# Kernel optimization log

Measured on AMD Instinct MI355X. Metric: run time of the kernel, lower is better.

The kernel has to match this reference:

```python
import jax, jax.numpy as jnp
import numpy as np

DIM = 2048
N_HEADS = 16
HEAD_DIM = DIM // N_HEADS
WINDOW = 256
B, S = 2, 2048


def setup_inputs() -> dict:
    key = jax.random.key(0)
    kx, kq, kk, kv, ko = jax.random.split(key, 5)
    bound = 1.0 / np.sqrt(DIM)  # nn.Linear default init range
    x = jax.random.normal(kx, (B, S, DIM), dtype=jnp.float32)
    wq = jax.random.uniform(kq, (DIM, DIM), jnp.float32, -bound, bound)
    wk = jax.random.uniform(kk, (DIM, DIM), jnp.float32, -bound, bound)
    wv = jax.random.uniform(kv, (DIM, DIM), jnp.float32, -bound, bound)
    wo = jax.random.uniform(ko, (DIM, DIM), jnp.float32, -bound, bound)
    return {"x": x, "wq": wq, "wk": wk, "wv": wv, "wo": wo}


def reference(x, wq, wk, wv, wo):
    b, s, d = x.shape
    scale = HEAD_DIM ** -0.5
    # projections (torch Linear: y = x @ W.T)
    q = (x @ wq.T).reshape(b, s, N_HEADS, HEAD_DIM)
    k = (x @ wk.T).reshape(b, s, N_HEADS, HEAD_DIM)
    v = (x @ wv.T).reshape(b, s, N_HEADS, HEAD_DIM)
    # scores: [b, h, i, j]
    scores = jnp.einsum("bihd,bjhd->bhij", q, k) * scale
    # faithful mask: (all-ones, window cleared, then triu(1)) == mask iff j - i > window//2
    idx = jnp.arange(s)
    mask = (idx[None, :] - idx[:, None]) > (WINDOW // 2)  # [s, s] bool, True = masked
    scores = jnp.where(mask[None, None, :, :], -jnp.inf, scores)
    attn = jax.nn.softmax(scores, axis=-1)
    out = jnp.einsum("bhij,bjhd->bihd", attn, v).reshape(b, s, d)
    return out @ wo.T
```

## Files before the change

### kernel.cpp

```cpp
#include <hip/hip_runtime.h>
#include <stdint.h>
#include <stddef.h>

#define DIMN 2048
#define NH 16
#define HD 128
#define SEQ 2048
#define WIN 128

typedef __attribute__((ext_vector_type(4))) float f32x4;
typedef __attribute__((ext_vector_type(8))) short bf16x8;
typedef __attribute__((ext_vector_type(4))) int i32x4;

#define AS1 __attribute__((address_space(1)))
#define AS3 __attribute__((address_space(3)))

__device__ __forceinline__ unsigned short f2bf(float f) {
  union { float f; unsigned u; } v; v.f = f;
  unsigned r = v.u + 0x7FFFu + ((v.u >> 16) & 1u);
  return (unsigned short)(r >> 16);
}

__global__ void cast_bf16_kernel(const float* __restrict__ src,
                                 unsigned short* __restrict__ dst, int n4) {
  int i = blockIdx.x * blockDim.x + threadIdx.x;
  const int stride = gridDim.x * blockDim.x;
  for (; i < n4; i += stride) {
    float4 v = ((const float4*)src)[i];
    ushort4 o;
    o.x = f2bf(v.x); o.y = f2bf(v.y); o.z = f2bf(v.z); o.w = f2bf(v.w);
    ((ushort4*)dst)[i] = o;
  }
}

__global__ void cast4_bf16_kernel(const float* __restrict__ s0, const float* __restrict__ s1,
                                  const float* __restrict__ s2, const float* __restrict__ s3,
                                  unsigned short* __restrict__ dst, int n4) {
  const float* s = (blockIdx.y == 0) ? s0 : (blockIdx.y == 1) ? s1 : (blockIdx.y == 2) ? s2 : s3;
  unsigned short* d = dst + (size_t)blockIdx.y * 4194304;
  int i = blockIdx.x * blockDim.x + threadIdx.x;
  const int stride = gridDim.x * blockDim.x;
  for (; i < n4; i += stride) {
    float4 v = ((const float4*)s)[i];
    ushort4 o;
    o.x = f2bf(v.x); o.y = f2bf(v.y); o.z = f2bf(v.z); o.w = f2bf(v.w);
    ((ushort4*)d)[i] = o;
  }
}

__device__ __forceinline__ void gemm_mainloop_g128(
    const unsigned short* __restrict__ A, const unsigned short* __restrict__ B,
    int m0, int n0, unsigned short* As, unsigned short* Bs, f32x4 acc[4][4]) {
  const int t = threadIdx.x, lane = t & 63, wid = t >> 6;
  const int c = lane & 15, g = lane >> 4;
  const int wr = wid >> 1, wc = wid & 1;

  const int srow = wid * 32 + (lane >> 3);
  const int gslot = (lane & 7) ^ (lane >> 3);
  const unsigned short* ga = A + (size_t)(m0 + srow) * DIMN + gslot * 8;
  const unsigned short* gb = B + (size_t)(n0 + srow) * DIMN + gslot * 8;
  unsigned short* la = As + (size_t)(wid * 32) * 64;
  unsigned short* lb = Bs + (size_t)(wid * 32) * 64;

  const int swc = c & 7;

  for (int k0 = 0; k0 < DIMN; k0 += 64) {
    __syncthreads();
#pragma unroll
    for (int i = 0; i < 4; ++i) {
      __builtin_amdgcn_global_load_lds(
          (const AS1 unsigned*)(ga + (size_t)i * 8 * DIMN + k0),
          (AS3 unsigned*)(la + i * 8 * 64), 16, 0, 0);
      __builtin_amdgcn_global_load_lds(
          (const AS1 unsigned*)(gb + (size_t)i * 8 * DIMN + k0),
          (AS3 unsigned*)(lb + i * 8 * 64), 16, 0, 0);
    }
    __syncthreads();
#pragma unroll
    for (int kk = 0; kk < 2; ++kk) {
      bf16x8 af[4], bfv[4];
#pragma unroll
      for (int mi = 0; mi < 4; ++mi)
        af[mi] = *(const bf16x8*)&As[(wr * 64 + mi * 16 + c) * 64 +
                                     (((kk * 4 + g) ^ swc) * 8)];
#pragma unroll
      for (int ni = 0; ni < 4; ++ni)
        bfv[ni] = *(const bf16x8*)&Bs[(wc * 64 + ni * 16 + c) * 64 +
                                      (((kk * 4 + g) ^ swc) * 8)];
#pragma unroll
      for (int mi = 0; mi < 4; ++mi)
#pragma unroll
        for (int ni = 0; ni < 4; ++ni)
          acc[mi][ni] = __builtin_amdgcn_mfma_f32_16x16x32_bf16(
              af[mi], bfv[ni], acc[mi][ni], 0, 0, 0);
    }
  }
}

__global__ __launch_bounds__(256, 3) void gemm_qkv_kernel(
    const unsigned short* __restrict__ Xb,
    const unsigned short* __restrict__ Wq,
    const unsigned short* __restrict__ Wk,
    const unsigned short* __restrict__ Wv,
    unsigned short* __restrict__ Qb,
    unsigned short* __restrict__ Kb,
    unsigned short* __restrict__ Vt) {
  __shared__ __attribute__((aligned(16))) unsigned short As[128 * 64];
  __shared__ __attribute__((aligned(16))) unsigned short Bs[128 * 64];
  const int z = blockIdx.z;
  const unsigned short* W = (z == 0) ? Wq : (z == 1) ? Wk : Wv;
  const int m0 = blockIdx.y * 128, n0 = blockIdx.x * 128;

  f32x4 acc[4][4];
  const f32x4 zv = {0.f, 0.f, 0.f, 0.f};
#pragma unroll
  for (int i = 0; i < 4; ++i)
#pragma unroll
    for (int j = 0; j < 4; ++j) acc[i][j] = zv;

  gemm_mainloop_g128(Xb, W, m0, n0, As, Bs, acc);

  const int lane = threadIdx.x & 63, wid = threadIdx.x >> 6;
  const int c = lane & 15, g = lane >> 4;
  const int wr = wid >> 1, wc = wid & 1;
  unsigned short* Out01 = (z == 0) ? Qb : Kb;
#pragma unroll
  for (int mi = 0; mi < 4; ++mi) {
#pragma unroll
    for (int ni = 0; ni < 4; ++ni) {
      const int mrow = m0 + wr * 64 + mi * 16 + g * 4;
      const int ncol = n0 + wc * 64 + ni * 16 + c;
      const int h = ncol >> 7, d = ncol & 127;
      const int b = mrow >> 11, s = mrow & 2047;
      if (z < 2) {
#pragma unroll
        for (int j = 0; j < 4; ++j)
          Out01[((size_t)(b * NH + h) * SEQ + s + j) * HD + d] =
              f2bf(acc[mi][ni][j]);
      } else {
        ushort4 pk;
        pk.x = f2bf(acc[mi][ni][0]); pk.y = f2bf(acc[mi][ni][1]);
        pk.z = f2bf(acc[mi][ni][2]); pk.w = f2bf(acc[mi][ni][3]);
        *(ushort4*)&Vt[((size_t)(b * NH + h) * HD + d) * SEQ + s] = pk;
      }
    }
  }
}

__global__ __launch_bounds__(256, 3) void gemm_out_kernel(
    const unsigned short* __restrict__ Ab,
    const unsigned short* __restrict__ Wo,
    float* __restrict__ Cf) {
  __shared__ __attribute__((aligned(16))) unsigned short As[128 * 64];
  __shared__ __attribute__((aligned(16))) unsigned short Bs[128 * 64];
  const int m0 = blockIdx.y * 128, n0 = blockIdx.x * 128;

  f32x4 acc[4][4];
  const f32x4 zv = {0.f, 0.f, 0.f, 0.f};
#pragma unroll
  for (int i = 0; i < 4; ++i)
#pragma unroll
    for (int j = 0; j < 4; ++j) acc[i][j] = zv;

  gemm_mainloop_g128(Ab, Wo, m0, n0, As, Bs, acc);

  const int lane = threadIdx.x & 63, wid = threadIdx.x >> 6;
  const int c = lane & 15, g = lane >> 4;
  const int wr = wid >> 1, wc = wid & 1;
#pragma unroll
  for (int mi = 0; mi < 4; ++mi) {
#pragma unroll
    for (int ni = 0; ni < 4; ++ni) {
      const int mrow = m0 + wr * 64 + mi * 16 + g * 4;
      const int ncol = n0 + wc * 64 + ni * 16 + c;
#pragma unroll
      for (int j = 0; j < 4; ++j)
        Cf[(size_t)(mrow + j) * DIMN + ncol] = acc[mi][ni][j];
    }
  }
}

__global__ __launch_bounds__(256, 2) void attn_kernel(
    const unsigned short* __restrict__ Qg,
    const unsigned short* __restrict__ Kg,
    const unsigned short* __restrict__ Vtg,
    unsigned short* __restrict__ Og) {
  __shared__ __attribute__((aligned(16))) unsigned short Ks[2][64 * 128];
  __shared__ __attribute__((aligned(16))) unsigned short Vs[2][128 * 64];
  __shared__ __attribute__((aligned(16))) unsigned short Ps[4 * 32 * 64];

  const int bh = blockIdx.x;
  const int yy = blockIdx.y;
  const int qt = (yy < 8) ? yy : 23 - yy;
  const int q0 = qt * 128;
  const int t = threadIdx.x, wid = t >> 6, lane = t & 63;
  const int c = lane & 15, g = lane >> 4;
  const int swc = c & 7;

  const unsigned short* Kbh = Kg + (size_t)bh * SEQ * HD;
  const unsigned short* Vbh = Vtg + (size_t)bh * HD * SEQ;

  bf16x8 qf[2][4];
#pragma unroll
  for (int mi = 0; mi < 2; ++mi) {
    const unsigned short* qb =
        Qg + ((size_t)bh * SEQ + q0 + wid * 32 + mi * 16 + c) * HD + g * 8;
#pragma unroll
    for (int kk = 0; kk < 4; ++kk) qf[mi][kk] = *(const bf16x8*)(qb + kk * 32);
  }

  f32x4 o[2][8];
  const f32x4 zv = {0.f, 0.f, 0.f, 0.f};
#pragma unroll
  for (int mi = 0; mi < 2; ++mi)
#pragma unroll
    for (int ni = 0; ni < 8; ++ni) o[mi][ni] = zv;
  float M[2][4], L[2][4];
#pragma unroll
  for (int mi = 0; mi < 2; ++mi)
#pragma unroll
    for (int j = 0; j < 4; ++j) { M[mi][j] = -1e30f; L[mi][j] = 0.f; }

  const int ntA = (q0 + 256) >> 6;
  const int nt = (ntA < (SEQ >> 6)) ? ntA : (SEQ >> 6);
  const float kl2e = 0.08838834764831845f * 1.4426950408889634f;

  const int kswz = (t & 15) ^ ((t >> 4) & 7);
  const int vswz = (t & 7) ^ ((t >> 3) & 7);
  const int kgo = (t >> 4) * HD + (t & 15) * 8;
  const int klo = (t >> 4) * 128 + kswz * 8;
  const int vlo = (t >> 3) * 64 + vswz * 8;
  const size_t vgo = (size_t)(t >> 3) * SEQ + (t & 7) * 8;

  i32x4 kc[4], vc[4];
#pragma unroll
  for (int r = 0; r < 4; ++r) {
    kc[r] = *(const i32x4*)(Kbh + (size_t)r * 16 * HD + kgo);
    vc[r] = *(const i32x4*)(Vbh + (size_t)r * 32 * SEQ + vgo);
  }
#pragma unroll
  for (int r = 0; r < 4; ++r) {
    *(i32x4*)&Ks[0][r * 2048 + klo] = kc[r];
    *(i32x4*)&Vs[0][r * 2048 + vlo] = vc[r];
  }
  if (nt > 1) {
#pragma unroll
    for (int r = 0; r < 4; ++r) {
      kc[r] = *(const i32x4*)(Kbh + (size_t)(64 + r * 16) * HD + kgo);
      vc[r] = *(const i32x4*)(Vbh + (size_t)r * 32 * SEQ + 64 + vgo);
    }
  }
  __syncthreads();

  int cur = 0;
  for (int tt = 0; tt < nt; ++tt) {
    const int j0 = tt * 64;
    if (tt + 1 < nt) {
#pragma unroll
      for (int r = 0; r < 4; ++r) {
        *(i32x4*)&Ks[cur ^ 1][r * 2048 + klo] = kc[r];
        *(i32x4*)&Vs[cur ^ 1][r * 2048 + vlo] = vc[r];
      }
      if (tt + 2 < nt) {
        const int j2 = j0 + 128;
#pragma unroll
        for (int r = 0; r < 4; ++r) {
          kc[r] = *(const i32x4*)(Kbh + (size_t)(j2 + r * 16) * HD + kgo);
          vc[r] = *(const i32x4*)(Vbh + (size_t)r * 32 * SEQ + j2 + vgo);
        }
      }
    }
    const unsigned short* Kc = Ks[cur];
    const unsigned short* Vc = Vs[cur];

    f32x4 sc[2][4];
#pragma unroll
    for (int mi = 0; mi < 2; ++mi)
#pragma unroll
      for (int ni = 0; ni < 4; ++ni) sc[mi][ni] = zv;
    __builtin_amdgcn_s_setprio(1);
#pragma unroll
    for (int kk = 0; kk < 4; ++kk) {
#pragma unroll
      for (int ni = 0; ni < 4; ++ni) {
        const bf16x8 kf =
            *(const bf16x8*)&Kc[(ni * 16 + c) * 128 + ((kk * 4 + g) ^ swc) * 8];
        sc[0][ni] = __builtin_amdgcn_mfma_f32_16x16x32_bf16(qf[0][kk], kf, sc[0][ni], 0, 0, 0);
        sc[1][ni] = __builtin_amdgcn_mfma_f32_16x16x32_bf16(qf[1][kk], kf, sc[1][ni], 0, 0, 0);
      }
    }
    __builtin_amdgcn_s_setprio(0);

    if (j0 - q0 >= 128) {
#pragma unroll
      for (int mi = 0; mi < 2; ++mi)
#pragma unroll
        for (int ni = 0; ni < 4; ++ni) {
          const int jg = j0 + ni * 16 + c;
#pragma unroll
          for (int j = 0; j < 4; ++j) {
            const int ig = q0 + wid * 32 + mi * 16 + g * 4 + j;
            if (jg > ig + WIN) sc[mi][ni][j] = -3.0e38f;
          }
        }
    }

    float tmax[2][4], dmax = -3.0e38f;
#pragma unroll
    for (int mi = 0; mi < 2; ++mi)
#pragma unroll
      for (int j = 0; j < 4; ++j) {
        float mx = fmaxf(fmaxf(sc[mi][0][j], sc[mi][1][j]),
                         fmaxf(sc[mi][2][j], sc[mi][3][j]));
        mx = fmaxf(mx, __shfl_xor(mx, 1));
        mx = fmaxf(mx, __shfl_xor(mx, 2));
        mx = fmaxf(mx, __shfl_xor(mx, 4));
        mx = fmaxf(mx, __shfl_xor(mx, 8));
        tmax[mi][j] = mx;
        dmax = fmaxf(dmax, mx - M[mi][j]);
      }
    if (__any(dmax > 64.f)) {
#pragma unroll
      for (int mi = 0; mi < 2; ++mi)
#pragma unroll
        for (int j = 0; j < 4; ++j) {
          const float nm = fmaxf(M[mi][j], tmax[mi][j]);
          const float al = __builtin_amdgcn_exp2f((M[mi][j] - nm) * kl2e);
          M[mi][j] = nm;
          L[mi][j] *= al;
#pragma unroll
          for (int ni = 0; ni < 8; ++ni) o[mi][ni][j] *= al;
        }
    }

#pragma unroll
    for (int mi = 0; mi < 2; ++mi) {
      float rs0 = 0.f, rs1 = 0.f, rs2 = 0.f, rs3 = 0.f;
#pragma unroll
      for (int ni = 0; ni < 4; ++ni)
#pragma unroll
        for (int j = 0; j < 4; ++j) {
          const float p = __builtin_amdgcn_exp2f((sc[mi][ni][j] - M[mi][j]) * kl2e);
          if (j == 0) rs0 += p; else if (j == 1) rs1 += p;
          else if (j == 2) rs2 += p; else rs3 += p;
          const int prow = mi * 16 + g * 4 + j;
          Ps[wid * 2048 + prow * 64 + ((2 * ni + (c >> 3)) ^ (prow & 7)) * 8 + (c & 7)] =
              f2bf(p);
        }
      L[mi][0] += rs0; L[mi][1] += rs1; L[mi][2] += rs2; L[mi][3] += rs3;
    }

    __builtin_amdgcn_s_setprio(1);
#pragma unroll
    for (int kk2 = 0; kk2 < 2; ++kk2) {
      bf16x8 pf[2];
#pragma unroll
      for (int mi = 0; mi < 2; ++mi)
        pf[mi] = *(const bf16x8*)&Ps[wid * 2048 + (mi * 16 + c) * 64 +
                                     ((kk2 * 4 + g) ^ swc) * 8];
#pragma unroll
      for (int ni = 0; ni < 8; ++ni) {
        const bf16x8 vf =
            *(const bf16x8*)&Vc[(ni * 16 + c) * 64 + ((kk2 * 4 + g) ^ swc) * 8];
        o[0][ni] = __builtin_amdgcn_mfma_f32_16x16x32_bf16(pf[0], vf, o[0][ni], 0, 0, 0);
        o[1][ni] = __builtin_amdgcn_mfma_f32_16x16x32_bf16(pf[1], vf, o[1][ni], 0, 0, 0);
      }
    }
    __builtin_amdgcn_s_setprio(0);

    __syncthreads();
    cur ^= 1;
  }

  const int b = bh >> 4, h = bh & 15;
#pragma unroll
  for (int mi = 0; mi < 2; ++mi)
#pragma unroll
    for (int j = 0; j < 4; ++j) {
      float s = L[mi][j];
      s += __shfl_xor(s, 1);
      s += __shfl_xor(s, 2);
      s += __shfl_xor(s, 4);
      s += __shfl_xor(s, 8);
      const float inv = 1.0f / s;
      const int srow = q0 + wid * 32 + mi * 16 + g * 4 + j;
      unsigned short* orow = Og + (size_t)(b * SEQ + srow) * DIMN + h * HD;
#pragma unroll
      for (int ni = 0; ni < 8; ++ni) orow[ni * 16 + c] = f2bf(o[mi][ni][j] * inv);
    }
}

extern "C" void kernel_launch(void* const* d_in, const int* in_sizes, int n_in,
                              void* d_out, int out_size, void* d_ws, size_t ws_size,
                              hipStream_t stream) {
  (void)in_sizes; (void)n_in; (void)out_size; (void)ws_size;
  const float* x  = (const float*)d_in[0];
  const float* wq = (const float*)d_in[1];
  const float* wk = (const float*)d_in[2];
  const float* wv = (const float*)d_in[3];
  const float* wo = (const float*)d_in[4];
  float* out = (float*)d_out;

  unsigned short* xb  = (unsigned short*)d_ws;
  unsigned short* wqb = xb  + (size_t)8388608;
  unsigned short* wkb = wqb + (size_t)4194304;
  unsigned short* wvb = wkb + (size_t)4194304;
  unsigned short* wob = wvb + (size_t)4194304;
  unsigned short* Qb  = wob + (size_t)4194304;
  unsigned short* Kb  = Qb  + (size_t)8388608;
  unsigned short* Vt  = Kb  + (size_t)8388608;
  unsigned short* Ab  = Vt  + (size_t)8388608;

  cast_bf16_kernel<<<dim3(1024), dim3(256), 0, stream>>>(x, xb, 2097152);
  cast4_bf16_kernel<<<dim3(512, 4), dim3(256), 0, stream>>>(wq, wk, wv, wo, wqb, 1048576);

  gemm_qkv_kernel<<<dim3(16, 32, 3), dim3(256), 0, stream>>>(xb, wqb, wkb, wvb, Qb, Kb, Vt);
  attn_kernel<<<dim3(32, 16), dim3(256), 0, stream>>>(Qb, Kb, Vt, Ab);
  gemm_out_kernel<<<dim3(16, 32), dim3(256), 0, stream>>>(Ab, wob, out);
}
```

Before: 379.3 us.

## Transpose attention MFMA operands so each lane owns a query row; merge cast kernels

Result: faster. 345.5 us (-8.9%).

```diff
diff --git a/kernel.cpp b/kernel.cpp
--- a/kernel.cpp
+++ b/kernel.cpp
@@ -21,30 +21,25 @@
   return (unsigned short)(r >> 16);
 }
 
-__global__ void cast_bf16_kernel(const float* __restrict__ src,
-                                 unsigned short* __restrict__ dst, int n4) {
+__global__ void cast_all_kernel(const float* __restrict__ x,
+                                const float* __restrict__ wq, const float* __restrict__ wk,
+                                const float* __restrict__ wv, const float* __restrict__ wo,
+                                unsigned short* __restrict__ dst) {
+  const int y = blockIdx.y;
+  const float* s;
+  if (y < 2) s = x + (size_t)y * 4194304;
+  else if (y == 2) s = wq;
+  else if (y == 3) s = wk;
+  else if (y == 4) s = wv;
+  else s = wo;
+  ushort4* d = (ushort4*)dst + (size_t)y * 1048576;
   int i = blockIdx.x * blockDim.x + threadIdx.x;
   const int stride = gridDim.x * blockDim.x;
-  for (; i < n4; i += stride) {
-    float4 v = ((const float4*)src)[i];
-    ushort4 o;
-    o.x = f2bf(v.x); o.y = f2bf(v.y); o.z = f2bf(v.z); o.w = f2bf(v.w);
-    ((ushort4*)dst)[i] = o;
-  }
-}
-
-__global__ void cast4_bf16_kernel(const float* __restrict__ s0, const float* __restrict__ s1,
-                                  const float* __restrict__ s2, const float* __restrict__ s3,
-                                  unsigned short* __restrict__ dst, int n4) {
-  const float* s = (blockIdx.y == 0) ? s0 : (blockIdx.y == 1) ? s1 : (blockIdx.y == 2) ? s2 : s3;
-  unsigned short* d = dst + (size_t)blockIdx.y * 4194304;
-  int i = blockIdx.x * blockDim.x + threadIdx.x;
-  const int stride = gridDim.x * blockDim.x;
-  for (; i < n4; i += stride) {
+  for (; i < 1048576; i += stride) {
     float4 v = ((const float4*)s)[i];
     ushort4 o;
     o.x = f2bf(v.x); o.y = f2bf(v.y); o.z = f2bf(v.z); o.w = f2bf(v.w);
-    ((ushort4*)d)[i] = o;
+    d[i] = o;
   }
 }
 
@@ -215,11 +210,8 @@
   for (int mi = 0; mi < 2; ++mi)
 #pragma unroll
     for (int ni = 0; ni < 8; ++ni) o[mi][ni] = zv;
-  float M[2][4], L[2][4];
-#pragma unroll
-  for (int mi = 0; mi < 2; ++mi)
-#pragma unroll
-    for (int j = 0; j < 4; ++j) { M[mi][j] = -1e30f; L[mi][j] = 0.f; }
+  float M[2] = {-1e30f, -1e30f};
+  float L[2] = {0.f, 0.f};
 
   const int ntA = (q0 + 256) >> 6;
   const int nt = (ntA < (SEQ >> 6)) ? ntA : (SEQ >> 6);
@@ -285,69 +277,68 @@
       for (int ni = 0; ni < 4; ++ni) {
         const bf16x8 kf =
             *(const bf16x8*)&Kc[(ni * 16 + c) * 128 + ((kk * 4 + g) ^ swc) * 8];
-        sc[0][ni] = __builtin_amdgcn_mfma_f32_16x16x32_bf16(qf[0][kk], kf, sc[0][ni], 0, 0, 0);
-        sc[1][ni] = __builtin_amdgcn_mfma_f32_16x16x32_bf16(qf[1][kk], kf, sc[1][ni], 0, 0, 0);
+        sc[0][ni] = __builtin_amdgcn_mfma_f32_16x16x32_bf16(kf, qf[0][kk], sc[0][ni], 0, 0, 0);
+        sc[1][ni] = __builtin_amdgcn_mfma_f32_16x16x32_bf16(kf, qf[1][kk], sc[1][ni], 0, 0, 0);
       }
     }
     __builtin_amdgcn_s_setprio(0);
 
     if (j0 - q0 >= 128) {
 #pragma unroll
-      for (int mi = 0; mi < 2; ++mi)
+      for (int mi = 0; mi < 2; ++mi) {
+        const int ig = q0 + wid * 32 + mi * 16 + c;
 #pragma unroll
         for (int ni = 0; ni < 4; ++ni) {
-          const int jg = j0 + ni * 16 + c;
 #pragma unroll
           for (int j = 0; j < 4; ++j) {
-            const int ig = q0 + wid * 32 + mi * 16 + g * 4 + j;
+            const int jg = j0 + ni * 16 + g * 4 + j;
             if (jg > ig + WIN) sc[mi][ni][j] = -3.0e38f;
           }
         }
-    }
-
-    float tmax[2][4], dmax = -3.0e38f;
-#pragma unroll
-    for (int mi = 0; mi < 2; ++mi)
-#pragma unroll
-      for (int j = 0; j < 4; ++j) {
-        float mx = fmaxf(fmaxf(sc[mi][0][j], sc[mi][1][j]),
-                         fmaxf(sc[mi][2][j], sc[mi][3][j]));
-        mx = fmaxf(mx, __shfl_xor(mx, 1));
-        mx = fmaxf(mx, __shfl_xor(mx, 2));
-        mx = fmaxf(mx, __shfl_xor(mx, 4));
-        mx = fmaxf(mx, __shfl_xor(mx, 8));
-        tmax[mi][j] = mx;
-        dmax = fmaxf(dmax, mx - M[mi][j]);
-      }
+      }
+    }
+
+    float tmax[2];
+#pragma unroll
+    for (int mi = 0; mi < 2; ++mi) {
+      float m0v = fmaxf(fmaxf(sc[mi][0][0], sc[mi][0][1]), fmaxf(sc[mi][0][2], sc[mi][0][3]));
+      float m1v = fmaxf(fmaxf(sc[mi][1][0], sc[mi][1][1]), fmaxf(sc[mi][1][2], sc[mi][1][3]));
+      float m2v = fmaxf(fmaxf(sc[mi][2][0], sc[mi][2][1]), fmaxf(sc[mi][2][2], sc[mi][2][3]));
+      float m3v = fmaxf(fmaxf(sc[mi][3][0], sc[mi][3][1]), fmaxf(sc[mi][3][2], sc[mi][3][3]));
+      float mx = fmaxf(fmaxf(m0v, m1v), fmaxf(m2v, m3v));
+      mx = fmaxf(mx, __shfl_xor(mx, 16));
+      mx = fmaxf(mx, __shfl_xor(mx, 32));
+      tmax[mi] = mx;
+    }
+    const float dmax = fmaxf(tmax[0] - M[0], tmax[1] - M[1]);
     if (__any(dmax > 64.f)) {
 #pragma unroll
-      for (int mi = 0; mi < 2; ++mi)
+      for (int mi = 0; mi < 2; ++mi) {
+        const float nm = fmaxf(M[mi], tmax[mi]);
+        const float al = __builtin_amdgcn_exp2f((M[mi] - nm) * kl2e);
+        M[mi] = nm;
+        L[mi] *= al;
+#pragma unroll
+        for (int ni = 0; ni < 8; ++ni) o[mi][ni] *= al;
+      }
+    }
+
+#pragma unroll
+    for (int mi = 0; mi < 2; ++mi) {
+      float rs = 0.f;
+#pragma unroll
+      for (int ni = 0; ni < 4; ++ni) {
+        ushort4 pk;
 #pragma unroll
         for (int j = 0; j < 4; ++j) {
-          const float nm = fmaxf(M[mi][j], tmax[mi][j]);
-          const float al = __builtin_amdgcn_exp2f((M[mi][j] - nm) * kl2e);
-          M[mi][j] = nm;
-          L[mi][j] *= al;
-#pragma unroll
-          for (int ni = 0; ni < 8; ++ni) o[mi][ni][j] *= al;
+          const float p = __builtin_amdgcn_exp2f((sc[mi][ni][j] - M[mi]) * kl2e);
+          rs += p;
+          ((unsigned short*)&pk)[j] = f2bf(p);
         }
-    }
-
-#pragma unroll
-    for (int mi = 0; mi < 2; ++mi) {
-      float rs0 = 0.f, rs1 = 0.f, rs2 = 0.f, rs3 = 0.f;
-#pragma unroll
-      for (int ni = 0; ni < 4; ++ni)
-#pragma unroll
-        for (int j = 0; j < 4; ++j) {
-          const float p = __builtin_amdgcn_exp2f((sc[mi][ni][j] - M[mi][j]) * kl2e);
-          if (j == 0) rs0 += p; else if (j == 1) rs1 += p;
-          else if (j == 2) rs2 += p; else rs3 += p;
-          const int prow = mi * 16 + g * 4 + j;
-          Ps[wid * 2048 + prow * 64 + ((2 * ni + (c >> 3)) ^ (prow & 7)) * 8 + (c & 7)] =
-              f2bf(p);
-        }
-      L[mi][0] += rs0; L[mi][1] += rs1; L[mi][2] += rs2; L[mi][3] += rs3;
+        *(ushort4*)&Ps[wid * 2048 + (mi * 16 + c) * 64 +
+                       ((2 * ni + (g >> 1)) ^ swc) * 8 + (g & 1) * 4] = pk;
+      }
+      L[mi] += rs;
     }
 
     __builtin_amdgcn_s_setprio(1);
@@ -362,8 +353,8 @@
       for (int ni = 0; ni < 8; ++ni) {
         const bf16x8 vf =
             *(const bf16x8*)&Vc[(ni * 16 + c) * 64 + ((kk2 * 4 + g) ^ swc) * 8];
-        o[0][ni] = __builtin_amdgcn_mfma_f32_16x16x32_bf16(pf[0], vf, o[0][ni], 0, 0, 0);
-        o[1][ni] = __builtin_amdgcn_mfma_f32_16x16x32_bf16(pf[1], vf, o[1][ni], 0, 0, 0);
+        o[0][ni] = __builtin_amdgcn_mfma_f32_16x16x32_bf16(vf, pf[0], o[0][ni], 0, 0, 0);
+        o[1][ni] = __builtin_amdgcn_mfma_f32_16x16x32_bf16(vf, pf[1], o[1][ni], 0, 0, 0);
       }
     }
     __builtin_amdgcn_s_setprio(0);
@@ -374,20 +365,23 @@
 
   const int b = bh >> 4, h = bh & 15;
 #pragma unroll
-  for (int mi = 0; mi < 2; ++mi)
-#pragma unroll
-    for (int j = 0; j < 4; ++j) {
-      float s = L[mi][j];
-      s += __shfl_xor(s, 1);
-      s += __shfl_xor(s, 2);
-      s += __shfl_xor(s, 4);
-      s += __shfl_xor(s, 8);
-      const float inv = 1.0f / s;
-      const int srow = q0 + wid * 32 + mi * 16 + g * 4 + j;
-      unsigned short* orow = Og + (size_t)(b * SEQ + srow) * DIMN + h * HD;
-#pragma unroll
-      for (int ni = 0; ni < 8; ++ni) orow[ni * 16 + c] = f2bf(o[mi][ni][j] * inv);
-    }
+  for (int mi = 0; mi < 2; ++mi) {
+    float s = L[mi];
+    s += __shfl_xor(s, 16);
+    s += __shfl_xor(s, 32);
+    const float inv = 1.0f / s;
+    const int q = q0 + wid * 32 + mi * 16 + c;
+    unsigned short* orow = Og + (size_t)(b * SEQ + q) * DIMN + h * HD;
+#pragma unroll
+    for (int ni = 0; ni < 8; ++ni) {
+      ushort4 pk;
+      pk.x = f2bf(o[mi][ni][0] * inv);
+      pk.y = f2bf(o[mi][ni][1] * inv);
+      pk.z = f2bf(o[mi][ni][2] * inv);
+      pk.w = f2bf(o[mi][ni][3] * inv);
+      *(ushort4*)&orow[ni * 16 + g * 4] = pk;
+    }
+  }
 }
 
 extern "C" void kernel_launch(void* const* d_in, const int* in_sizes, int n_in,
@@ -411,8 +405,7 @@
   unsigned short* Vt  = Kb  + (size_t)8388608;
   unsigned short* Ab  = Vt  + (size_t)8388608;
 
-  cast_bf16_kernel<<<dim3(1024), dim3(256), 0, stream>>>(x, xb, 2097152);
-  cast4_bf16_kernel<<<dim3(512, 4), dim3(256), 0, stream>>>(wq, wk, wv, wo, wqb, 1048576);
+  cast_all_kernel<<<dim3(512, 6), dim3(256), 0, stream>>>(x, wq, wk, wv, wo, xb);
 
   gemm_qkv_kernel<<<dim3(16, 32, 3), dim3(256), 0, stream>>>(xb, wqb, wkb, wvb, Qb, Kb, Vt);
   attn_kernel<<<dim3(32, 16), dim3(256), 0, stream>>>(Qb, Kb, Vt, Ab);
```
